# Optimization experiments

Measured on AMD Instinct MI355X. Metric: run time of the kernel, lower is better.

## Reference

```python
import jax, jax.numpy as jnp
import numpy as np

N_NODES = 100000
N_EDGES = 1600000
D_IN = 64
D_OUT = 64


def setup_inputs() -> dict:
    key = jax.random.key(0)
    ks = jax.random.split(key, 8)
    x = jax.random.normal(ks[0], (N_NODES, D_IN), dtype=jnp.float32)
    edge_rows = jax.random.randint(ks[1], (N_EDGES,), 0, N_NODES, dtype=jnp.int32)
    edge_cols = jax.random.randint(ks[2], (N_EDGES,), 0, N_NODES, dtype=jnp.int32)
    edge_vals = jax.random.uniform(ks[3], (N_EDGES,), dtype=jnp.float32)
    # xavier_uniform with gain=2.0: limit = gain * sqrt(6 / (fan_in + fan_out))
    lim = 2.0 * float(np.sqrt(6.0 / (D_IN + D_OUT)))
    weight_own = jax.random.uniform(ks[4], (D_IN, D_OUT), jnp.float32, -lim, lim)
    weight_nbr = jax.random.uniform(ks[5], (D_IN, D_OUT), jnp.float32, -lim, lim)
    weight_temp = jax.random.uniform(ks[6], (D_IN, D_OUT), jnp.float32, -lim, lim)
    bias = jnp.zeros((D_OUT,), jnp.float32)
    return {
        "x": x,
        "edge_rows": edge_rows,
        "edge_cols": edge_cols,
        "edge_vals": edge_vals,
        "weight_own": weight_own,
        "weight_nbr": weight_nbr,
        "weight_temp": weight_temp,
        "bias": bias,
    }


def _spmm(edge_rows, edge_cols, edge_vals, dense):
    # COO sparse [N,N] @ dense [N,D]: gather source rows, scale by edge value,
    # scatter-add into destination rows.
    msgs = edge_vals[:, None] * dense[edge_cols]  # [E, D]
    return jax.ops.segment_sum(msgs, edge_rows, num_segments=N_NODES)


def reference(x, edge_rows, edge_cols, edge_vals, weight_own, weight_nbr, weight_temp, bias):
    support = x @ weight_own    # [N, D_OUT]
    support1 = x @ weight_nbr
    support2 = x @ weight_temp
    output = _spmm(edge_rows, edge_cols, edge_vals, support)
    output1 = _spmm(edge_rows, edge_cols, edge_vals, support1)
    output2 = _spmm(edge_rows, edge_cols, edge_vals, support2)
    return output + output1 + output2 + bias
```

## Files before the change

kernel.cpp:

```cpp
#include <hip/hip_runtime.h>
#include <hip/hip_bf16.h>

#define D 64
#define RPB 256
#define RSH 8
#define NBMAX 1024
#define CPAD 16

__global__ __launch_bounds__(256) void gemm_kernel(const float* __restrict__ x,
                                                   const float* __restrict__ w0,
                                                   const float* __restrict__ w1,
                                                   const float* __restrict__ w2,
                                                   __hip_bfloat16* __restrict__ support,
                                                   int n) {
    __shared__ float Ws[D * D];
    __shared__ float xs[4][D];

    for (int i = threadIdx.x; i < D * D; i += 256)
        Ws[i] = w0[i] + w1[i] + w2[i];
    __syncthreads();

    const int wid  = threadIdx.x >> 6;
    const int lane = threadIdx.x & 63;
    int row = blockIdx.x * 4 + wid;
    const int nw = gridDim.x * 4;

    for (; row < n; row += nw) {
        xs[wid][lane] = x[(size_t)row * D + lane];
        float acc = 0.0f;
#pragma unroll
        for (int k = 0; k < D; ++k) {
            acc += xs[wid][k] * Ws[k * D + lane];
        }
        support[(size_t)row * D + lane] = __float2bfloat16(acc);
    }
}

__global__ __launch_bounds__(256) void gemm_f32_kernel(const float* __restrict__ x,
                                                       const float* __restrict__ w0,
                                                       const float* __restrict__ w1,
                                                       const float* __restrict__ w2,
                                                       float* __restrict__ support,
                                                       int n) {
    __shared__ float Ws[D * D];
    __shared__ float xs[4][D];
    for (int i = threadIdx.x; i < D * D; i += 256)
        Ws[i] = w0[i] + w1[i] + w2[i];
    __syncthreads();
    const int wid  = threadIdx.x >> 6;
    const int lane = threadIdx.x & 63;
    int row = blockIdx.x * 4 + wid;
    const int nw = gridDim.x * 4;
    for (; row < n; row += nw) {
        xs[wid][lane] = x[(size_t)row * D + lane];
        float acc = 0.0f;
#pragma unroll
        for (int k = 0; k < D; ++k) acc += xs[wid][k] * Ws[k * D + lane];
        support[(size_t)row * D + lane] = acc;
    }
}

__global__ __launch_bounds__(256) void zero_kernel(int* __restrict__ p, int n) {
    int i = blockIdx.x * 256 + threadIdx.x;
    int stride = gridDim.x * 256;
    for (; i < n; i += stride) p[i] = 0;
}

__global__ __launch_bounds__(256) void bucket_hist_kernel(const int* __restrict__ rows,
                                                          int ne, int* __restrict__ gcnt,
                                                          int nb) {
    __shared__ int lcnt[NBMAX];
    for (int i = threadIdx.x; i < nb; i += 256) lcnt[i] = 0;
    __syncthreads();
    int i = blockIdx.x * 256 + threadIdx.x;
    int stride = gridDim.x * 256;
    for (; i < ne; i += stride) atomicAdd(&lcnt[rows[i] >> RSH], 1);
    __syncthreads();
    for (int b = threadIdx.x; b < nb; b += 256) {
        int c = lcnt[b];
        if (c) atomicAdd(&gcnt[b * CPAD], c);
    }
}

__global__ __launch_bounds__(256) void bucket_scan_kernel(const int* __restrict__ gcnt,
                                                          int nb,
                                                          int* __restrict__ base,
                                                          int* __restrict__ cursor) {
    __shared__ int ts[256];
    const int tid = threadIdx.x;
    int b0 = tid * 4;
    int v[4]; int tsum = 0;
#pragma unroll
    for (int j = 0; j < 4; ++j) {
        int idx = b0 + j;
        v[j] = (idx < nb) ? gcnt[idx * CPAD] : 0;
        tsum += v[j];
    }
    ts[tid] = tsum;
    __syncthreads();
    for (int off = 1; off < 256; off <<= 1) {
        int t = (tid >= off) ? ts[tid - off] : 0;
        __syncthreads();
        ts[tid] += t;
        __syncthreads();
    }
    int excl = ts[tid] - tsum;
#pragma unroll
    for (int j = 0; j < 4; ++j) {
        int idx = b0 + j;
        if (idx < nb) { base[idx] = excl; cursor[idx * CPAD] = excl; }
        excl += v[j];
    }
    if (tid == 255) base[nb] = excl;
}

__global__ __launch_bounds__(256) void bin_scatter_kernel(const int* __restrict__ rows,
                                                          const int* __restrict__ cols,
                                                          const float* __restrict__ vals,
                                                          int ne,
                                                          int* __restrict__ cursor,
                                                          int nb,
                                                          int2* __restrict__ binned) {
    __shared__ int lcnt[NBMAX];
    __shared__ int lbase[NBMAX];
    const int tid = threadIdx.x;
    const int ce = (ne + gridDim.x - 1) / gridDim.x;
    const int e0 = blockIdx.x * ce;
    const int e1 = min(ne, e0 + ce);

    for (int i = tid; i < nb; i += 256) lcnt[i] = 0;
    __syncthreads();
    for (int e = e0 + tid; e < e1; e += 256) atomicAdd(&lcnt[rows[e] >> RSH], 1);
    __syncthreads();
    for (int b = tid; b < nb; b += 256) {
        int c = lcnt[b];
        lbase[b] = c ? atomicAdd(&cursor[b * CPAD], c) : 0;
    }
    __syncthreads();
    for (int i = tid; i < nb; i += 256) lcnt[i] = 0;
    __syncthreads();
    for (int e = e0 + tid; e < e1; e += 256) {
        int r = rows[e];
        int b = r >> RSH;
        int loc = atomicAdd(&lcnt[b], 1);
        int2 cv;
        cv.x = ((r & (RPB - 1)) << 17) | cols[e];
        cv.y = __float_as_int(vals[e]);
        binned[lbase[b] + loc] = cv;
    }
}

__global__ __launch_bounds__(512) void local_csr_kernel(const int* __restrict__ base,
                                                        const int2* __restrict__ binned,
                                                        int* __restrict__ rowptr,
                                                        int2* __restrict__ csr,
                                                        int n) {
    __shared__ int lh[RPB];
    __shared__ int lp[RPB];
    const int tid = threadIdx.x;
    const int b = blockIdx.x;
    const int jb = base[b], je = base[b + 1];

    for (int i = tid; i < RPB; i += 512) lh[i] = 0;
    __syncthreads();
    for (int j = jb + tid; j < je; j += 512) atomicAdd(&lh[binned[j].x >> 17], 1);
    __syncthreads();
    if (tid < RPB) lp[tid] = lh[tid];
    __syncthreads();
    for (int off = 1; off < RPB; off <<= 1) {
        int t = (tid < RPB && tid >= off) ? lp[tid - off] : 0;
        __syncthreads();
        if (tid < RPB) lp[tid] += t;
        __syncthreads();
    }
    if (tid < RPB) {
        int excl = lp[tid] - lh[tid];
        int start = jb + excl;
        lh[tid] = start;
        int r = b * RPB + tid;
        if (r < n) rowptr[r] = start;
    }
    __syncthreads();
    for (int j = jb + tid; j < je; j += 512) {
        int2 e = binned[j];
        int rl = e.x >> 17;
        int pos = atomicAdd(&lh[rl], 1);
        int2 o; o.x = e.x & 0x1FFFF; o.y = e.y;
        csr[pos] = o;
    }
}

__global__ __launch_bounds__(256) void pull2_kernel(const int* __restrict__ rowptr,
                                                    const int2* __restrict__ csr,
                                                    const unsigned int* __restrict__ sup32,
                                                    const float* __restrict__ bias,
                                                    float* __restrict__ out, int n) {
    const int tid  = threadIdx.x;
    const int lane = tid & 63;
    const int half = lane >> 5;
    const int sub  = lane & 31;
    const int wave = blockIdx.x * 4 + (tid >> 6);
    const int nwave = gridDim.x * 4;
    const float2 b2 = reinterpret_cast<const float2*>(bias)[sub];

    for (int w = wave; 2 * w < n; w += nwave) {
        const int r = 2 * w + half;
        float ax = 0.0f, ay = 0.0f;
        if (r < n) {
            int jb = rowptr[r], je = rowptr[r + 1];
            int j = jb;
            for (; j + 3 < je; j += 4) {
                int2 e0 = csr[j], e1 = csr[j + 1], e2 = csr[j + 2], e3 = csr[j + 3];
                unsigned int u0 = sup32[(size_t)e0.x * 32 + sub];
                unsigned int u1 = sup32[(size_t)e1.x * 32 + sub];
                unsigned int u2 = sup32[(size_t)e2.x * 32 + sub];
                unsigned int u3 = sup32[(size_t)e3.x * 32 + sub];
                float v0 = __int_as_float(e0.y), v1 = __int_as_float(e1.y);
                float v2 = __int_as_float(e2.y), v3 = __int_as_float(e3.y);
                ax += v0 * __uint_as_float(u0 << 16);
                ay += v0 * __uint_as_float(u0 & 0xffff0000u);
                ax += v1 * __uint_as_float(u1 << 16);
                ay += v1 * __uint_as_float(u1 & 0xffff0000u);
                ax += v2 * __uint_as_float(u2 << 16);
                ay += v2 * __uint_as_float(u2 & 0xffff0000u);
                ax += v3 * __uint_as_float(u3 << 16);
                ay += v3 * __uint_as_float(u3 & 0xffff0000u);
            }
            for (; j < je; ++j) {
                int2 e = csr[j];
                unsigned int u = sup32[(size_t)e.x * 32 + sub];
                float v = __int_as_float(e.y);
                ax += v * __uint_as_float(u << 16);
                ay += v * __uint_as_float(u & 0xffff0000u);
            }
            float2 o; o.x = ax + b2.x; o.y = ay + b2.y;
            reinterpret_cast<float2*>(out)[(size_t)r * 32 + sub] = o;
        }
    }
}

__global__ __launch_bounds__(256) void init_kernel(const float* __restrict__ bias,
                                                   float* __restrict__ out, int total4) {
    int i = blockIdx.x * 256 + threadIdx.x;
    int stride = gridDim.x * 256;
    for (; i < total4; i += stride) {
        int base4 = (i * 4) & (D - 1);
        float4 bv;
        bv.x = bias[base4 + 0]; bv.y = bias[base4 + 1];
        bv.z = bias[base4 + 2]; bv.w = bias[base4 + 3];
        reinterpret_cast<float4*>(out)[i] = bv;
    }
}

__global__ __launch_bounds__(256) void scatter_kernel(const int* __restrict__ rows,
                                                      const int* __restrict__ cols,
                                                      const float* __restrict__ vals,
                                                      const float* __restrict__ support,
                                                      float* __restrict__ out, int ne) {
    const int wid  = blockIdx.x * 4 + (threadIdx.x >> 6);
    const int lane = threadIdx.x & 63;
    const int nw = gridDim.x * 4;
    for (int e = wid; e < ne; e += nw) {
        const int r = rows[e];
        const int c = cols[e];
        const float v = vals[e];
        unsafeAtomicAdd(&out[(size_t)r * D + lane], v * support[(size_t)c * D + lane]);
    }
}

extern "C" void kernel_launch(void* const* d_in, const int* in_sizes, int n_in,
                              void* d_out, int out_size, void* d_ws, size_t ws_size,
                              hipStream_t stream) {
    const float* x         = (const float*)d_in[0];
    const int*   edge_rows = (const int*)d_in[1];
    const int*   edge_cols = (const int*)d_in[2];
    const float* edge_vals = (const float*)d_in[3];
    const float* w_own     = (const float*)d_in[4];
    const float* w_nbr     = (const float*)d_in[5];
    const float* w_temp    = (const float*)d_in[6];
    const float* bias      = (const float*)d_in[7];

    float* out = (float*)d_out;
    const int n_nodes = in_sizes[0] / D;
    const int n_edges = in_sizes[1];
    const int nb = (n_nodes + RPB - 1) / RPB;

    char* ws = (char*)d_ws;
    size_t off = 0;
    auto take = [&](size_t bytes) -> char* {
        char* p = ws + off;
        off = (off + bytes + 15) & ~(size_t)15;
        return p;
    };
    __hip_bfloat16* support = (__hip_bfloat16*)take((size_t)n_nodes * D * sizeof(__hip_bfloat16));
    int2* binned = (int2*)take((size_t)n_edges * sizeof(int2));
    int2* csr    = (int2*)take((size_t)n_edges * sizeof(int2));
    int*  rowptr = (int*) take((size_t)(n_nodes + 1) * sizeof(int));
    int*  gcnt   = (int*) take((size_t)nb * CPAD * sizeof(int));
    int*  base   = (int*) take((size_t)(nb + 1) * sizeof(int));
    int*  cursor = (int*) take((size_t)nb * CPAD * sizeof(int));
    const bool full_fits = (off <= ws_size) && (nb <= NBMAX) && (n_nodes <= (1 << 17));

    if (full_fits) {
        gemm_kernel<<<1024, 256, 0, stream>>>(x, w_own, w_nbr, w_temp, support, n_nodes);
        zero_kernel<<<32, 256, 0, stream>>>(gcnt, nb * CPAD);
        bucket_hist_kernel<<<512, 256, 0, stream>>>(edge_rows, n_edges, gcnt, nb);
        bucket_scan_kernel<<<1, 256, 0, stream>>>(gcnt, nb, base, cursor);
        bin_scatter_kernel<<<512, 256, 0, stream>>>(edge_rows, edge_cols, edge_vals,
                                                    n_edges, cursor, nb, binned);
        local_csr_kernel<<<nb, 512, 0, stream>>>(base, binned, rowptr, csr, n_nodes);
        hipMemcpyAsync(rowptr + n_nodes, base + nb, sizeof(int),
                       hipMemcpyDeviceToDevice, stream);
        pull2_kernel<<<2048, 256, 0, stream>>>(rowptr, csr, (const unsigned int*)support,
                                               bias, out, n_nodes);
    } else {
        float* support_f = (float*)d_ws;
        gemm_f32_kernel<<<1024, 256, 0, stream>>>(x, w_own, w_nbr, w_temp, support_f, n_nodes);
        int total4 = (n_nodes * D) / 4;
        int blocks = (total4 + 255) / 256; if (blocks > 2048) blocks = 2048;
        init_kernel<<<blocks, 256, 0, stream>>>(bias, out, total4);
        scatter_kernel<<<2048, 256, 0, stream>>>(edge_rows, edge_cols, edge_vals,
                                                 support_f, out, n_edges);
    }
}
```

Measured before the change: 139.2 us.

## Split edge binning into two-level radix scatter (super-bucket then sub-bucket)

Replaces the single-pass scatter of edges into ~391 row buckets with two passes. The first pass scatters into up to 32 super-buckets, and the second redistributes each super-bucket into 32 sub-buckets. This is meant to improve write locality and cut the per-block work over 1024-entry shared histograms, at the cost of an extra full read/write pass over the edge array. It also doubles the histogram grid and reuses the first binned buffer as the CSR output.

```diff
diff --git a/kernel.cpp b/kernel.cpp
--- a/kernel.cpp
+++ b/kernel.cpp
@@ -4,7 +4,9 @@
 #define D 64
 #define RPB 256
 #define RSH 8
+#define SSH 13
 #define NBMAX 1024
+#define NSMAX 32
 #define CPAD 16
 
 __global__ __launch_bounds__(256) void gemm_kernel(const float* __restrict__ x,
@@ -83,9 +85,11 @@
 }
 
 __global__ __launch_bounds__(256) void bucket_scan_kernel(const int* __restrict__ gcnt,
-                                                          int nb,
+                                                          int nb, int ns,
                                                           int* __restrict__ base,
-                                                          int* __restrict__ cursor) {
+                                                          int* __restrict__ cursor,
+                                                          int* __restrict__ sbase,
+                                                          int* __restrict__ scursor) {
     __shared__ int ts[256];
     const int tid = threadIdx.x;
     int b0 = tid * 4;
@@ -108,45 +112,92 @@
 #pragma unroll
     for (int j = 0; j < 4; ++j) {
         int idx = b0 + j;
-        if (idx < nb) { base[idx] = excl; cursor[idx * CPAD] = excl; }
+        if (idx < nb) {
+            base[idx] = excl;
+            cursor[idx * CPAD] = excl;
+            if ((idx & 31) == 0) {
+                int ss = idx >> 5;
+                sbase[ss] = excl;
+                scursor[ss * CPAD] = excl;
+            }
+        }
         excl += v[j];
     }
-    if (tid == 255) base[nb] = excl;
-}
-
-__global__ __launch_bounds__(256) void bin_scatter_kernel(const int* __restrict__ rows,
-                                                          const int* __restrict__ cols,
-                                                          const float* __restrict__ vals,
-                                                          int ne,
-                                                          int* __restrict__ cursor,
-                                                          int nb,
-                                                          int2* __restrict__ binned) {
-    __shared__ int lcnt[NBMAX];
-    __shared__ int lbase[NBMAX];
+    if (tid == 255) { base[nb] = excl; sbase[ns] = excl; }
+}
+
+__global__ __launch_bounds__(256) void super_scatter_kernel(const int* __restrict__ rows,
+                                                            const int* __restrict__ cols,
+                                                            const float* __restrict__ vals,
+                                                            int ne, int ns,
+                                                            int* __restrict__ scursor,
+                                                            int2* __restrict__ binnedA) {
+    __shared__ int lcnt[NSMAX];
+    __shared__ int lbase[NSMAX];
     const int tid = threadIdx.x;
     const int ce = (ne + gridDim.x - 1) / gridDim.x;
     const int e0 = blockIdx.x * ce;
     const int e1 = min(ne, e0 + ce);
 
-    for (int i = tid; i < nb; i += 256) lcnt[i] = 0;
-    __syncthreads();
-    for (int e = e0 + tid; e < e1; e += 256) atomicAdd(&lcnt[rows[e] >> RSH], 1);
-    __syncthreads();
-    for (int b = tid; b < nb; b += 256) {
-        int c = lcnt[b];
-        lbase[b] = c ? atomicAdd(&cursor[b * CPAD], c) : 0;
-    }
-    __syncthreads();
-    for (int i = tid; i < nb; i += 256) lcnt[i] = 0;
+    for (int i = tid; i < ns; i += 256) lcnt[i] = 0;
+    __syncthreads();
+    for (int e = e0 + tid; e < e1; e += 256) atomicAdd(&lcnt[rows[e] >> SSH], 1);
+    __syncthreads();
+    if (tid < ns) {
+        int c = lcnt[tid];
+        lbase[tid] = c ? atomicAdd(&scursor[tid * CPAD], c) : 0;
+    }
+    __syncthreads();
+    for (int i = tid; i < ns; i += 256) lcnt[i] = 0;
     __syncthreads();
     for (int e = e0 + tid; e < e1; e += 256) {
         int r = rows[e];
-        int b = r >> RSH;
-        int loc = atomicAdd(&lcnt[b], 1);
+        int s = r >> SSH;
+        int loc = atomicAdd(&lcnt[s], 1);
         int2 cv;
-        cv.x = ((r & (RPB - 1)) << 17) | cols[e];
+        cv.x = ((r & 8191) << 17) | cols[e];
         cv.y = __float_as_int(vals[e]);
-        binned[lbase[b] + loc] = cv;
+        binnedA[lbase[s] + loc] = cv;
+    }
+}
+
+__global__ __launch_bounds__(256) void sub_scatter_kernel(const int2* __restrict__ binnedA,
+                                                          const int* __restrict__ sbase,
+                                                          int nb,
+                                                          int* __restrict__ cursor,
+                                                          int2* __restrict__ binnedB) {
+    __shared__ int lcnt[32];
+    __shared__ int lbase[32];
+    const int tid = threadIdx.x;
+    const int s = blockIdx.x >> 5;
+    const int i = blockIdx.x & 31;
+    const int e0s = sbase[s], e1s = sbase[s + 1];
+    const int chunk = ((e1s - e0s) + 31) >> 5;
+    const int e0 = e0s + i * chunk;
+    const int e1 = min(e1s, e0 + chunk);
+
+    if (tid < 32) lcnt[tid] = 0;
+    __syncthreads();
+    for (int e = e0 + tid; e < e1; e += 256)
+        atomicAdd(&lcnt[binnedA[e].x >> (17 + RSH)], 1);
+    __syncthreads();
+    if (tid < 32) {
+        int c = lcnt[tid];
+        int b = (s << 5) + tid;
+        lbase[tid] = c ? atomicAdd(&cursor[b * CPAD], c) : 0;
+    }
+    __syncthreads();
+    if (tid < 32) lcnt[tid] = 0;
+    __syncthreads();
+    for (int e = e0 + tid; e < e1; e += 256) {
+        int2 u = binnedA[e];
+        int rsl = u.x >> 17;
+        int sub = rsl >> RSH;
+        int loc = atomicAdd(&lcnt[sub], 1);
+        int2 o;
+        o.x = ((rsl & (RPB - 1)) << 17) | (u.x & 0x1FFFF);
+        o.y = u.y;
+        binnedB[lbase[sub] + loc] = o;
     }
 }
 
@@ -284,6 +335,7 @@
     const int n_nodes = in_sizes[0] / D;
     const int n_edges = in_sizes[1];
     const int nb = (n_nodes + RPB - 1) / RPB;
+    const int ns = (nb + 31) >> 5;
 
     char* ws = (char*)d_ws;
     size_t off = 0;
@@ -293,22 +345,27 @@
         return p;
     };
     __hip_bfloat16* support = (__hip_bfloat16*)take((size_t)n_nodes * D * sizeof(__hip_bfloat16));
-    int2* binned = (int2*)take((size_t)n_edges * sizeof(int2));
-    int2* csr    = (int2*)take((size_t)n_edges * sizeof(int2));
-    int*  rowptr = (int*) take((size_t)(n_nodes + 1) * sizeof(int));
-    int*  gcnt   = (int*) take((size_t)nb * CPAD * sizeof(int));
-    int*  base   = (int*) take((size_t)(nb + 1) * sizeof(int));
-    int*  cursor = (int*) take((size_t)nb * CPAD * sizeof(int));
-    const bool full_fits = (off <= ws_size) && (nb <= NBMAX) && (n_nodes <= (1 << 17));
+    int2* binnedA = (int2*)take((size_t)n_edges * sizeof(int2));
+    int2* binnedB = (int2*)take((size_t)n_edges * sizeof(int2));
+    int*  rowptr  = (int*) take((size_t)(n_nodes + 1) * sizeof(int));
+    int*  gcnt    = (int*) take((size_t)nb * CPAD * sizeof(int));
+    int*  base    = (int*) take((size_t)(nb + 1) * sizeof(int));
+    int*  cursor  = (int*) take((size_t)nb * CPAD * sizeof(int));
+    int*  sbase   = (int*) take((size_t)(ns + 1) * sizeof(int));
+    int*  scursor = (int*) take((size_t)ns * CPAD * sizeof(int));
+    int2* csr     = binnedA;
+    const bool full_fits = (off <= ws_size) && (nb <= NBMAX) && (ns <= NSMAX) &&
+                           (n_nodes <= (1 << 17));
 
     if (full_fits) {
         gemm_kernel<<<1024, 256, 0, stream>>>(x, w_own, w_nbr, w_temp, support, n_nodes);
         zero_kernel<<<32, 256, 0, stream>>>(gcnt, nb * CPAD);
-        bucket_hist_kernel<<<512, 256, 0, stream>>>(edge_rows, n_edges, gcnt, nb);
-        bucket_scan_kernel<<<1, 256, 0, stream>>>(gcnt, nb, base, cursor);
-        bin_scatter_kernel<<<512, 256, 0, stream>>>(edge_rows, edge_cols, edge_vals,
-                                                    n_edges, cursor, nb, binned);
-        local_csr_kernel<<<nb, 512, 0, stream>>>(base, binned, rowptr, csr, n_nodes);
+        bucket_hist_kernel<<<1024, 256, 0, stream>>>(edge_rows, n_edges, gcnt, nb);
+        bucket_scan_kernel<<<1, 256, 0, stream>>>(gcnt, nb, ns, base, cursor, sbase, scursor);
+        super_scatter_kernel<<<1024, 256, 0, stream>>>(edge_rows, edge_cols, edge_vals,
+                                                       n_edges, ns, scursor, binnedA);
+        sub_scatter_kernel<<<ns * 32, 256, 0, stream>>>(binnedA, sbase, nb, cursor, binnedB);
+        local_csr_kernel<<<nb, 512, 0, stream>>>(base, binnedB, rowptr, csr, n_nodes);
         hipMemcpyAsync(rowptr + n_nodes, base + nb, sizeof(int),
                        hipMemcpyDeviceToDevice, stream);
         pull2_kernel<<<2048, 256, 0, stream>>>(rowptr, csr, (const unsigned int*)support,
```

After: 158.6 us. 13.9% more time.

## Fuse local CSR build into pull kernel using shared-memory per-bucket edge staging

Applied to the files above, without the earlier changes.

Replaces the separate local_csr_kernel and pull2_kernel with one kernel. Two blocks share each 256-row bucket, one per half. Each block sorts its half's edges into shared memory in chunks and accumulates 16 rows per wave in registers. This removes the global CSR array, the rowptr write/read and one kernel launch plus a memcpy. The cost is that each block reads the whole bucket's binned edges twice and discards half. There are extra syncs, fewer blocks (nb*2), and 32 accumulator registers per thread. The bucket histogram grid is also doubled.

```diff
diff --git a/kernel.cpp b/kernel.cpp
--- a/kernel.cpp
+++ b/kernel.cpp
@@ -4,6 +4,8 @@
 #define D 64
 #define RPB 256
 #define RSH 8
+#define FPB 128
+#define CAP 2560
 #define NBMAX 1024
 #define CPAD 16
 
@@ -150,90 +152,97 @@
     }
 }
 
-__global__ __launch_bounds__(512) void local_csr_kernel(const int* __restrict__ base,
-                                                        const int2* __restrict__ binned,
-                                                        int* __restrict__ rowptr,
-                                                        int2* __restrict__ csr,
-                                                        int n) {
-    __shared__ int lh[RPB];
-    __shared__ int lp[RPB];
-    const int tid = threadIdx.x;
-    const int b = blockIdx.x;
-    const int jb = base[b], je = base[b + 1];
-
-    for (int i = tid; i < RPB; i += 512) lh[i] = 0;
-    __syncthreads();
-    for (int j = jb + tid; j < je; j += 512) atomicAdd(&lh[binned[j].x >> 17], 1);
-    __syncthreads();
-    if (tid < RPB) lp[tid] = lh[tid];
-    __syncthreads();
-    for (int off = 1; off < RPB; off <<= 1) {
-        int t = (tid < RPB && tid >= off) ? lp[tid - off] : 0;
-        __syncthreads();
-        if (tid < RPB) lp[tid] += t;
-        __syncthreads();
-    }
-    if (tid < RPB) {
-        int excl = lp[tid] - lh[tid];
-        int start = jb + excl;
-        lh[tid] = start;
-        int r = b * RPB + tid;
-        if (r < n) rowptr[r] = start;
-    }
-    __syncthreads();
-    for (int j = jb + tid; j < je; j += 512) {
-        int2 e = binned[j];
-        int rl = e.x >> 17;
-        int pos = atomicAdd(&lh[rl], 1);
-        int2 o; o.x = e.x & 0x1FFFF; o.y = e.y;
-        csr[pos] = o;
-    }
-}
-
-__global__ __launch_bounds__(256) void pull2_kernel(const int* __restrict__ rowptr,
-                                                    const int2* __restrict__ csr,
-                                                    const unsigned int* __restrict__ sup32,
-                                                    const float* __restrict__ bias,
-                                                    float* __restrict__ out, int n) {
+__global__ __launch_bounds__(256) void fused_pull_kernel(const int* __restrict__ base,
+                                                         const int2* __restrict__ binned,
+                                                         const unsigned int* __restrict__ sup32,
+                                                         const float* __restrict__ bias,
+                                                         float* __restrict__ out, int n) {
+    __shared__ int2 eds[CAP];
+    __shared__ int hist[FPB];
+    __shared__ int pref[FPB];
+    __shared__ int cur[FPB];
+
     const int tid  = threadIdx.x;
+    const int b    = blockIdx.x >> 1;
+    const int hi   = blockIdx.x & 1;
+    const int jb   = base[b], je = base[b + 1];
+    const int row0 = b * RPB + hi * FPB;
+
     const int lane = tid & 63;
+    const int wv   = tid >> 6;
     const int half = lane >> 5;
     const int sub  = lane & 31;
-    const int wave = blockIdx.x * 4 + (tid >> 6);
-    const int nwave = gridDim.x * 4;
     const float2 b2 = reinterpret_cast<const float2*>(bias)[sub];
 
-    for (int w = wave; 2 * w < n; w += nwave) {
-        const int r = 2 * w + half;
-        float ax = 0.0f, ay = 0.0f;
-        if (r < n) {
-            int jb = rowptr[r], je = rowptr[r + 1];
-            int j = jb;
-            for (; j + 3 < je; j += 4) {
-                int2 e0 = csr[j], e1 = csr[j + 1], e2 = csr[j + 2], e3 = csr[j + 3];
+    float ax[16], ay[16];
+#pragma unroll
+    for (int t = 0; t < 16; ++t) { ax[t] = 0.0f; ay[t] = 0.0f; }
+
+    for (int c0 = jb; c0 < je; c0 += CAP) {
+        const int c1 = min(je, c0 + CAP);
+
+        for (int i = tid; i < FPB; i += 256) hist[i] = 0;
+        __syncthreads();
+        for (int j = c0 + tid; j < c1; j += 256) {
+            int rl = binned[j].x >> 17;
+            if ((rl >> 7) == hi) atomicAdd(&hist[rl & (FPB - 1)], 1);
+        }
+        __syncthreads();
+
+        if (tid < FPB) pref[tid] = hist[tid];
+        __syncthreads();
+        for (int off = 1; off < FPB; off <<= 1) {
+            int t = (tid < FPB && tid >= off) ? pref[tid - off] : 0;
+            __syncthreads();
+            if (tid < FPB) pref[tid] += t;
+            __syncthreads();
+        }
+        if (tid < FPB) cur[tid] = pref[tid] - hist[tid];
+        __syncthreads();
+
+        for (int j = c0 + tid; j < c1; j += 256) {
+            int2 e = binned[j];
+            int rl = e.x >> 17;
+            if ((rl >> 7) == hi) {
+                int pos = atomicAdd(&cur[rl & (FPB - 1)], 1);
+                int2 o; o.x = e.x & 0x1FFFF; o.y = e.y;
+                eds[pos] = o;
+            }
+        }
+        __syncthreads();
+
+#pragma unroll
+        for (int t = 0; t < 16; ++t) {
+            const int rl = wv * 32 + 2 * t + half;
+            const int js = pref[rl] - hist[rl];
+            const int jeL = pref[rl];
+            int j = js;
+            for (; j + 1 < jeL; j += 2) {
+                int2 e0 = eds[j], e1 = eds[j + 1];
                 unsigned int u0 = sup32[(size_t)e0.x * 32 + sub];
                 unsigned int u1 = sup32[(size_t)e1.x * 32 + sub];
-                unsigned int u2 = sup32[(size_t)e2.x * 32 + sub];
-                unsigned int u3 = sup32[(size_t)e3.x * 32 + sub];
                 float v0 = __int_as_float(e0.y), v1 = __int_as_float(e1.y);
-                float v2 = __int_as_float(e2.y), v3 = __int_as_float(e3.y);
-                ax += v0 * __uint_as_float(u0 << 16);
-                ay += v0 * __uint_as_float(u0 & 0xffff0000u);
-                ax += v1 * __uint_as_float(u1 << 16);
-                ay += v1 * __uint_as_float(u1 & 0xffff0000u);
-                ax += v2 * __uint_as_float(u2 << 16);
-                ay += v2 * __uint_as_float(u2 & 0xffff0000u);
-                ax += v3 * __uint_as_float(u3 << 16);
-                ay += v3 * __uint_as_float(u3 & 0xffff0000u);
+                ax[t] += v0 * __uint_as_float(u0 << 16);
+                ay[t] += v0 * __uint_as_float(u0 & 0xffff0000u);
+                ax[t] += v1 * __uint_as_float(u1 << 16);
+                ay[t] += v1 * __uint_as_float(u1 & 0xffff0000u);
             }
-            for (; j < je; ++j) {
-                int2 e = csr[j];
+            if (j < jeL) {
+                int2 e = eds[j];
                 unsigned int u = sup32[(size_t)e.x * 32 + sub];
                 float v = __int_as_float(e.y);
-                ax += v * __uint_as_float(u << 16);
-                ay += v * __uint_as_float(u & 0xffff0000u);
+                ax[t] += v * __uint_as_float(u << 16);
+                ay[t] += v * __uint_as_float(u & 0xffff0000u);
             }
-            float2 o; o.x = ax + b2.x; o.y = ay + b2.y;
+        }
+        __syncthreads();
+    }
+
+#pragma unroll
+    for (int t = 0; t < 16; ++t) {
+        int r = row0 + wv * 32 + 2 * t + half;
+        if (r < n) {
+            float2 o; o.x = ax[t] + b2.x; o.y = ay[t] + b2.y;
             reinterpret_cast<float2*>(out)[(size_t)r * 32 + sub] = o;
         }
     }
@@ -294,8 +303,6 @@
     };
     __hip_bfloat16* support = (__hip_bfloat16*)take((size_t)n_nodes * D * sizeof(__hip_bfloat16));
     int2* binned = (int2*)take((size_t)n_edges * sizeof(int2));
-    int2* csr    = (int2*)take((size_t)n_edges * sizeof(int2));
-    int*  rowptr = (int*) take((size_t)(n_nodes + 1) * sizeof(int));
     int*  gcnt   = (int*) take((size_t)nb * CPAD * sizeof(int));
     int*  base   = (int*) take((size_t)(nb + 1) * sizeof(int));
     int*  cursor = (int*) take((size_t)nb * CPAD * sizeof(int));
@@ -304,15 +311,13 @@
     if (full_fits) {
         gemm_kernel<<<1024, 256, 0, stream>>>(x, w_own, w_nbr, w_temp, support, n_nodes);
         zero_kernel<<<32, 256, 0, stream>>>(gcnt, nb * CPAD);
-        bucket_hist_kernel<<<512, 256, 0, stream>>>(edge_rows, n_edges, gcnt, nb);
+        bucket_hist_kernel<<<1024, 256, 0, stream>>>(edge_rows, n_edges, gcnt, nb);
         bucket_scan_kernel<<<1, 256, 0, stream>>>(gcnt, nb, base, cursor);
         bin_scatter_kernel<<<512, 256, 0, stream>>>(edge_rows, edge_cols, edge_vals,
                                                     n_edges, cursor, nb, binned);
-        local_csr_kernel<<<nb, 512, 0, stream>>>(base, binned, rowptr, csr, n_nodes);
-        hipMemcpyAsync(rowptr + n_nodes, base + nb, sizeof(int),
-                       hipMemcpyDeviceToDevice, stream);
-        pull2_kernel<<<2048, 256, 0, stream>>>(rowptr, csr, (const unsigned int*)support,
-                                               bias, out, n_nodes);
+        fused_pull_kernel<<<nb * 2, 256, 0, stream>>>(base, binned,
+                                                      (const unsigned int*)support,
+                                                      bias, out, n_nodes);
     } else {
         float* support_f = (float*)d_ws;
         gemm_f32_kernel<<<1024, 256, 0, stream>>>(x, w_own, w_nbr, w_temp, support_f, n_nodes);
```

Result: slower. 183.1 us (+31.5%).

## Sort edges by bucket in shared memory before coalesced bin scatter

Applied to the files above, without the earlier changes.

The bin scatter kernel now stages each chunk of edges in LDS. It does a local count, scan and placement by bucket, then writes the edges to global memory in bucket-contiguous order so stores coalesce instead of scattering per edge. The zero kernel is replaced by a memset, the histogram grid is doubled, and the bucket limit is reduced to 512. The cost is extra LDS work, a block-wide scan with many barriers per chunk, and a per-element binary search to find each element's bucket.

```diff
diff --git a/kernel.cpp b/kernel.cpp
--- a/kernel.cpp
+++ b/kernel.cpp
@@ -4,8 +4,9 @@
 #define D 64
 #define RPB 256
 #define RSH 8
-#define NBMAX 1024
+#define NBMAX 512
 #define CPAD 16
+#define CAP 3200
 
 __global__ __launch_bounds__(256) void gemm_kernel(const float* __restrict__ x,
                                                    const float* __restrict__ w0,
@@ -60,12 +61,6 @@
     }
 }
 
-__global__ __launch_bounds__(256) void zero_kernel(int* __restrict__ p, int n) {
-    int i = blockIdx.x * 256 + threadIdx.x;
-    int stride = gridDim.x * 256;
-    for (; i < n; i += stride) p[i] = 0;
-}
-
 __global__ __launch_bounds__(256) void bucket_hist_kernel(const int* __restrict__ rows,
                                                           int ne, int* __restrict__ gcnt,
                                                           int nb) {
@@ -88,14 +83,10 @@
                                                           int* __restrict__ cursor) {
     __shared__ int ts[256];
     const int tid = threadIdx.x;
-    int b0 = tid * 4;
-    int v[4]; int tsum = 0;
-#pragma unroll
-    for (int j = 0; j < 4; ++j) {
-        int idx = b0 + j;
-        v[j] = (idx < nb) ? gcnt[idx * CPAD] : 0;
-        tsum += v[j];
-    }
+    int b0 = tid * 2;
+    int v0 = (b0 < nb)     ? gcnt[b0 * CPAD]       : 0;
+    int v1 = (b0 + 1 < nb) ? gcnt[(b0 + 1) * CPAD] : 0;
+    int tsum = v0 + v1;
     ts[tid] = tsum;
     __syncthreads();
     for (int off = 1; off < 256; off <<= 1) {
@@ -105,48 +96,75 @@
         __syncthreads();
     }
     int excl = ts[tid] - tsum;
-#pragma unroll
-    for (int j = 0; j < 4; ++j) {
-        int idx = b0 + j;
-        if (idx < nb) { base[idx] = excl; cursor[idx * CPAD] = excl; }
-        excl += v[j];
-    }
-    if (tid == 255) base[nb] = excl;
-}
-
-__global__ __launch_bounds__(256) void bin_scatter_kernel(const int* __restrict__ rows,
-                                                          const int* __restrict__ cols,
-                                                          const float* __restrict__ vals,
-                                                          int ne,
-                                                          int* __restrict__ cursor,
-                                                          int nb,
-                                                          int2* __restrict__ binned) {
-    __shared__ int lcnt[NBMAX];
-    __shared__ int lbase[NBMAX];
+    if (b0 < nb)     { base[b0] = excl;          cursor[b0 * CPAD] = excl; }
+    if (b0 + 1 < nb) { base[b0 + 1] = excl + v0; cursor[(b0 + 1) * CPAD] = excl + v0; }
+    if (tid == 255) base[nb] = excl + tsum;
+}
+
+__global__ __launch_bounds__(256) void bin_sort_scatter_kernel(const int* __restrict__ rows,
+                                                               const int* __restrict__ cols,
+                                                               const float* __restrict__ vals,
+                                                               int ne,
+                                                               int* __restrict__ cursor,
+                                                               int nb,
+                                                               int2* __restrict__ binned) {
+    __shared__ int2 sorted[CAP];
+    __shared__ int  pref[NBMAX];
+    __shared__ int  cur[NBMAX];
+    __shared__ int  lbase[NBMAX];
+    __shared__ int  ts[256];
     const int tid = threadIdx.x;
     const int ce = (ne + gridDim.x - 1) / gridDim.x;
     const int e0 = blockIdx.x * ce;
     const int e1 = min(ne, e0 + ce);
 
-    for (int i = tid; i < nb; i += 256) lcnt[i] = 0;
-    __syncthreads();
-    for (int e = e0 + tid; e < e1; e += 256) atomicAdd(&lcnt[rows[e] >> RSH], 1);
-    __syncthreads();
-    for (int b = tid; b < nb; b += 256) {
-        int c = lcnt[b];
-        lbase[b] = c ? atomicAdd(&cursor[b * CPAD], c) : 0;
-    }
-    __syncthreads();
-    for (int i = tid; i < nb; i += 256) lcnt[i] = 0;
-    __syncthreads();
-    for (int e = e0 + tid; e < e1; e += 256) {
-        int r = rows[e];
-        int b = r >> RSH;
-        int loc = atomicAdd(&lcnt[b], 1);
-        int2 cv;
-        cv.x = ((r & (RPB - 1)) << 17) | cols[e];
-        cv.y = __float_as_int(vals[e]);
-        binned[lbase[b] + loc] = cv;
+    for (int c0 = e0; c0 < e1; c0 += CAP) {
+        const int c1 = min(e1, c0 + CAP);
+        const int cnt = c1 - c0;
+
+        pref[2 * tid] = 0; pref[2 * tid + 1] = 0;
+        __syncthreads();
+        for (int e = c0 + tid; e < c1; e += 256)
+            atomicAdd(&pref[rows[e] >> RSH], 1);
+        __syncthreads();
+
+        int a0 = pref[2 * tid], a1 = pref[2 * tid + 1];
+        int tsum = a0 + a1;
+        ts[tid] = tsum;
+        __syncthreads();
+        for (int off = 1; off < 256; off <<= 1) {
+            int t = (tid >= off) ? ts[tid - off] : 0;
+            __syncthreads();
+            ts[tid] += t;
+            __syncthreads();
+        }
+        int excl = ts[tid] - tsum;
+        pref[2 * tid] = excl;           pref[2 * tid + 1] = excl + a0;
+        cur[2 * tid]  = excl;           cur[2 * tid + 1]  = excl + a0;
+        lbase[2 * tid]     = a0 ? atomicAdd(&cursor[(2 * tid) * CPAD], a0) : 0;
+        lbase[2 * tid + 1] = a1 ? atomicAdd(&cursor[(2 * tid + 1) * CPAD], a1) : 0;
+        __syncthreads();
+
+        for (int e = c0 + tid; e < c1; e += 256) {
+            int r = rows[e];
+            int b = r >> RSH;
+            int pos = atomicAdd(&cur[b], 1);
+            int2 cv;
+            cv.x = ((r & (RPB - 1)) << 17) | cols[e];
+            cv.y = __float_as_int(vals[e]);
+            sorted[pos] = cv;
+        }
+        __syncthreads();
+
+        for (int i = tid; i < cnt; i += 256) {
+            int lo = 0, hi = NBMAX - 1;
+            while (lo < hi) {
+                int mid = (lo + hi) >> 1;
+                if (cur[mid] > i) hi = mid; else lo = mid + 1;
+            }
+            binned[lbase[lo] + (i - pref[lo])] = sorted[i];
+        }
+        __syncthreads();
     }
 }
 
@@ -303,11 +321,11 @@
 
     if (full_fits) {
         gemm_kernel<<<1024, 256, 0, stream>>>(x, w_own, w_nbr, w_temp, support, n_nodes);
-        zero_kernel<<<32, 256, 0, stream>>>(gcnt, nb * CPAD);
-        bucket_hist_kernel<<<512, 256, 0, stream>>>(edge_rows, n_edges, gcnt, nb);
+        hipMemsetAsync(gcnt, 0, (size_t)nb * CPAD * sizeof(int), stream);
+        bucket_hist_kernel<<<1024, 256, 0, stream>>>(edge_rows, n_edges, gcnt, nb);
         bucket_scan_kernel<<<1, 256, 0, stream>>>(gcnt, nb, base, cursor);
-        bin_scatter_kernel<<<512, 256, 0, stream>>>(edge_rows, edge_cols, edge_vals,
-                                                    n_edges, cursor, nb, binned);
+        bin_sort_scatter_kernel<<<512, 256, 0, stream>>>(edge_rows, edge_cols, edge_vals,
+                                                         n_edges, cursor, nb, binned);
         local_csr_kernel<<<nb, 512, 0, stream>>>(base, binned, rowptr, csr, n_nodes);
         hipMemcpyAsync(rowptr + n_nodes, base + nb, sizeof(int),
                        hipMemcpyDeviceToDevice, stream);
```

New measurement: 151.9 us. 9.1% more time.
